# Optimization experiments

Measured on AMD Instinct MI355X. Metric: run time of the kernel, lower is better.

## Reference

```python
import jax, jax.numpy as jnp
import numpy as np

N = 50000      # num nodes
E = 800000     # num directed edges (before self loops)
C_IN = 128     # input channels
HID = 128      # hidden channels per head
H = 2          # attention heads (layer 0)
NEG_SLOPE = 0.2


def setup_inputs() -> dict:
    key = jax.random.key(0)
    ks = jax.random.split(key, 10)
    s = 0.05
    return {
        "x": jax.random.normal(ks[0], (N, C_IN), jnp.float32),
        "edge_index": jax.random.randint(ks[1], (2, E), 0, N, dtype=jnp.int32),
        "W1": jax.random.normal(ks[2], (C_IN, H * HID), jnp.float32) * s,
        "att_src1": jax.random.normal(ks[3], (H, HID), jnp.float32) * s,
        "att_dst1": jax.random.normal(ks[4], (H, HID), jnp.float32) * s,
        "b1": jax.random.normal(ks[5], (H * HID,), jnp.float32) * s,
        "W2": jax.random.normal(ks[6], (H * HID, 1), jnp.float32) * s,
        "att_src2": jax.random.normal(ks[7], (1, 1), jnp.float32) * s,
        "att_dst2": jax.random.normal(ks[8], (1, 1), jnp.float32) * s,
        "b2": jax.random.normal(ks[9], (1,), jnp.float32) * s,
    }


def gat_layer(x, src, dst, W, att_src, att_dst, bias, heads, out_ch, concat, num_nodes):
    # linear projection -> [N, H, C]
    h = (x @ W).reshape(num_nodes, heads, out_ch)
    a_src = jnp.einsum("nhc,hc->nh", h, att_src)  # [N, H]
    a_dst = jnp.einsum("nhc,hc->nh", h, att_dst)  # [N, H]
    # edge attention logits, LeakyReLU as in GATConv
    alpha = jax.nn.leaky_relu(a_src[src] + a_dst[dst], NEG_SLOPE)  # [Etot, H]
    # segment softmax over incoming edges of each destination node
    amax = jax.ops.segment_max(alpha, dst, num_segments=num_nodes)
    amax = jnp.where(jnp.isfinite(amax), amax, 0.0)
    ex = jnp.exp(alpha - amax[dst])
    denom = jax.ops.segment_sum(ex, dst, num_segments=num_nodes)
    coef = ex / (denom[dst] + 1e-16)                      # [Etot, H]
    # weighted scatter-aggregate of source features
    msg = h[src] * coef[:, :, None]                       # [Etot, H, C]
    out = jax.ops.segment_sum(msg, dst, num_segments=num_nodes)  # [N, H, C]
    out = out.reshape(num_nodes, heads * out_ch) if concat else out.mean(axis=1)
    return out + bias


def reference(x, edge_index, W1, att_src1, att_dst1, b1, W2, att_src2, att_dst2, b2):
    n = x.shape[0]
    loops = jnp.arange(n, dtype=edge_index.dtype)
    src = jnp.concatenate([edge_index[0], loops])  # GATConv adds self-loops
    dst = jnp.concatenate([edge_index[1], loops])
    h = gat_layer(x, src, dst, W1, att_src1, att_dst1, b1, H, HID, True, n)
    h = jax.nn.relu(h)
    out = gat_layer(h, src, dst, W2, att_src2, att_dst2, b2, 1, 1, False, n)
    return jax.nn.sigmoid(out)  # [N, 1]
```

## Files before the change

### kernel.cpp

```cpp
#include <hip/hip_runtime.h>
#include <hip/hip_bf16.h>

#define NEG_SLOPE 0.2f
#define MAXDEG 64

using f16x8 = __attribute__((ext_vector_type(8))) _Float16;
using f32x4 = __attribute__((ext_vector_type(4))) float;

__device__ inline unsigned short f2bf(float f) {
  __hip_bfloat16 b = __float2bfloat16(f);
  return __builtin_bit_cast(unsigned short, b);
}
__device__ inline unsigned short f2h(float f) {
  return __builtin_bit_cast(unsigned short, (_Float16)f);
}
__device__ inline float h2f(unsigned short u) {
  return (float)__builtin_bit_cast(_Float16, u);
}

__global__ __launch_bounds__(256) void k_pre(
    const float* __restrict__ W1, _Float16* __restrict__ W1T,
    int* __restrict__ cnt, int N) {
  const int b = blockIdx.x, t = threadIdx.x;
  if (b < 128) {
    const int e = b * 256 + t;
    const int k = e >> 8, c = e & 255;
    W1T[c * 128 + k] = (_Float16)W1[e];
  } else {
    const int i = (b - 128) * 256 + t;
    if (i < N) cnt[i] = 0;
  }
}

__global__ __launch_bounds__(256) void k1_mfma(
    const float* __restrict__ x, const _Float16* __restrict__ W1T,
    const float* __restrict__ att_src, const float* __restrict__ att_dst,
    _Float16* __restrict__ h1f, float4* __restrict__ attn, int N) {
  __shared__ _Float16 xs[64][136];
  const int t = threadIdx.x;
  const int w = t >> 6, l = t & 63;
  const int n0 = blockIdx.x * 64;

  {
    const int col4 = (t & 31) * 4;
#pragma unroll
    for (int p = 0; p < 8; ++p) {
      const int row = p * 8 + (t >> 5);
      float4 xv = make_float4(0.f, 0.f, 0.f, 0.f);
      if (n0 + row < N) xv = *(const float4*)(x + (size_t)(n0 + row) * 128 + col4);
      ushort4 u;
      u.x = f2h(xv.x); u.y = f2h(xv.y); u.z = f2h(xv.z); u.w = f2h(xv.w);
      *(ushort4*)&xs[row][col4] = u;
    }
  }
  __syncthreads();

  f32x4 acc[16];
#pragma unroll
  for (int nf = 0; nf < 16; ++nf) acc[nf] = f32x4{0.f, 0.f, 0.f, 0.f};
  const int cb = l & 15;
  const int kof = (l >> 4) * 8;
  const int xr = w * 16 + cb;
#pragma unroll
  for (int kk = 0; kk < 4; ++kk) {
    const f16x8 bx = *(const f16x8*)&xs[xr][kk * 32 + kof];
#pragma unroll
    for (int nf = 0; nf < 16; ++nf) {
      const f16x8 aw = *(const f16x8*)(W1T + (size_t)(nf * 16 + cb) * 128 + kk * 32 + kof);
      acc[nf] = __builtin_amdgcn_mfma_f32_16x16x32_f16(aw, bx, acc[nf], 0, 0, 0);
    }
  }

  const int node = n0 + w * 16 + cb;
  const int cg = (l >> 4) * 4;
  if (node < N) {
#pragma unroll
    for (int nf = 0; nf < 16; ++nf) {
      ushort4 u;
      u.x = f2h(acc[nf][0]); u.y = f2h(acc[nf][1]);
      u.z = f2h(acc[nf][2]); u.w = f2h(acc[nf][3]);
      *(ushort4*)(h1f + (size_t)node * 256 + nf * 16 + cg) = u;
    }
  }

  float s0 = 0.f, s1 = 0.f, d0 = 0.f, d1 = 0.f;
#pragma unroll
  for (int nf = 0; nf < 16; ++nf) {
    const float4 av = *(const float4*)(att_src + nf * 16 + cg);
    const float4 dv = *(const float4*)(att_dst + nf * 16 + cg);
    const float ls = acc[nf][0] * av.x + acc[nf][1] * av.y + acc[nf][2] * av.z + acc[nf][3] * av.w;
    const float ld = acc[nf][0] * dv.x + acc[nf][1] * dv.y + acc[nf][2] * dv.z + acc[nf][3] * dv.w;
    if (nf < 8) { s0 += ls; d0 += ld; } else { s1 += ls; d1 += ld; }
  }
  s0 += __shfl_xor(s0, 16); s0 += __shfl_xor(s0, 32);
  s1 += __shfl_xor(s1, 16); s1 += __shfl_xor(s1, 32);
  d0 += __shfl_xor(d0, 16); d0 += __shfl_xor(d0, 32);
  d1 += __shfl_xor(d1, 16); d1 += __shfl_xor(d1, 32);
  if (l < 16 && node < N) attn[node] = make_float4(s0, s1, d0, d1);
}

__global__ __launch_bounds__(256) void k_scatter(
    const int* __restrict__ ei, int E, int Etot,
    const float4* __restrict__ attn, int* __restrict__ cnt,
    int2* __restrict__ rec) {
  const int e = blockIdx.x * 256 + threadIdx.x;
  if (e >= Etot) return;
  int s, d;
  if (e < E) { s = ei[e]; d = ei[E + e]; } else { s = e - E; d = s; }
  const int slot = atomicAdd(&cnt[d], 1);
  if (slot >= MAXDEG) return;
  const float4 as = attn[s];
  const float4 ad = attn[d];
  float a0 = as.x + ad.z;
  float a1 = as.y + ad.w;
  a0 = a0 > 0.f ? a0 : a0 * NEG_SLOPE;
  a1 = a1 > 0.f ? a1 : a1 * NEG_SLOPE;
  const unsigned int wp = ((unsigned)f2bf(__expf(a1)) << 16) | f2bf(__expf(a0));
  rec[(size_t)d * MAXDEG + slot] = make_int2(s, (int)wp);
}

__global__ __launch_bounds__(256) void k3_gather(
    const int* __restrict__ cnt, const int2* __restrict__ rec,
    const _Float16* __restrict__ h1f,
    const float* __restrict__ b1, const float* __restrict__ W2,
    float* __restrict__ h2, int N) {
  const int wave = threadIdx.x >> 6, lane = threadIdx.x & 63;
  const int n = blockIdx.x * 4 + wave;
  if (n >= N) return;
  const bool hi = lane >= 32;
  const int deg = cnt[n];
  const int kcnt = deg < MAXDEG ? deg : MAXDEG;
  float4 acc = {0.f, 0.f, 0.f, 0.f};
  float den = 0.f;
  const unsigned short* h1u = (const unsigned short*)h1f;

  int sv = 0, wp = 0;
  if (lane < kcnt) {
    const int2 rv = rec[(size_t)n * MAXDEG + lane];
    sv = rv.x;
    wp = rv.y;
  }

  int s0_ = __shfl(sv, 0), s1_ = __shfl(sv, 1), s2_ = __shfl(sv, 2), s3_ = __shfl(sv, 3);
  ushort4 h0 = ((const ushort4*)(h1u + (size_t)s0_ * 256))[lane];
  ushort4 h1 = ((const ushort4*)(h1u + (size_t)s1_ * 256))[lane];
  ushort4 h2v = ((const ushort4*)(h1u + (size_t)s2_ * 256))[lane];
  ushort4 h3 = ((const ushort4*)(h1u + (size_t)s3_ * 256))[lane];

  for (int i = 0; i < kcnt; i += 4) {
    const int j0 = (i + 4) & 63, j1 = (i + 5) & 63, j2 = (i + 6) & 63, j3 = (i + 7) & 63;
    const int t0 = __shfl(sv, j0), t1 = __shfl(sv, j1), t2 = __shfl(sv, j2), t3 = __shfl(sv, j3);
    const ushort4 g0 = ((const ushort4*)(h1u + (size_t)t0 * 256))[lane];
    const ushort4 g1 = ((const ushort4*)(h1u + (size_t)t1 * 256))[lane];
    const ushort4 g2 = ((const ushort4*)(h1u + (size_t)t2 * 256))[lane];
    const ushort4 g3 = ((const ushort4*)(h1u + (size_t)t3 * 256))[lane];

    const unsigned int wp0 = (unsigned)__shfl(wp, i);
    const unsigned int wp1 = (unsigned)__shfl(wp, i + 1);
    const unsigned int wp2 = (unsigned)__shfl(wp, i + 2);
    const unsigned int wp3 = (unsigned)__shfl(wp, i + 3);
    const float w0 = __uint_as_float(hi ? (wp0 & 0xffff0000u) : (wp0 << 16));
    const float w1 = __uint_as_float(hi ? (wp1 & 0xffff0000u) : (wp1 << 16));
    const float w2 = __uint_as_float(hi ? (wp2 & 0xffff0000u) : (wp2 << 16));
    const float w3 = __uint_as_float(hi ? (wp3 & 0xffff0000u) : (wp3 << 16));

    acc.x = fmaf(h2f(h0.x), w0, acc.x); acc.y = fmaf(h2f(h0.y), w0, acc.y);
    acc.z = fmaf(h2f(h0.z), w0, acc.z); acc.w = fmaf(h2f(h0.w), w0, acc.w);
    acc.x = fmaf(h2f(h1.x), w1, acc.x); acc.y = fmaf(h2f(h1.y), w1, acc.y);
    acc.z = fmaf(h2f(h1.z), w1, acc.z); acc.w = fmaf(h2f(h1.w), w1, acc.w);
    acc.x = fmaf(h2f(h2v.x), w2, acc.x); acc.y = fmaf(h2f(h2v.y), w2, acc.y);
    acc.z = fmaf(h2f(h2v.z), w2, acc.z); acc.w = fmaf(h2f(h2v.w), w2, acc.w);
    acc.x = fmaf(h2f(h3.x), w3, acc.x); acc.y = fmaf(h2f(h3.y), w3, acc.y);
    acc.z = fmaf(h2f(h3.z), w3, acc.z); acc.w = fmaf(h2f(h3.w), w3, acc.w);
    den += w0 + w1 + w2 + w3;

    h0 = g0; h1 = g1; h2v = g2; h3 = g3;
  }

  const float inv = 1.f / (den + 1e-16f);
  const float4 bv = ((const float4*)b1)[lane];
  const float4 wv4 = ((const float4*)W2)[lane];
  float p = 0.f;
  p += fmaxf(fmaf(acc.x, inv, bv.x), 0.f) * wv4.x;
  p += fmaxf(fmaf(acc.y, inv, bv.y), 0.f) * wv4.y;
  p += fmaxf(fmaf(acc.z, inv, bv.z), 0.f) * wv4.z;
  p += fmaxf(fmaf(acc.w, inv, bv.w), 0.f) * wv4.w;
  for (int m = 32; m; m >>= 1) p += __shfl_xor(p, m);
  if (lane == 0) h2[n] = p;
}

__global__ __launch_bounds__(256) void k_l2(
    const int* __restrict__ cnt, const int2* __restrict__ rec,
    const float* __restrict__ h2,
    const float* __restrict__ att_s2, const float* __restrict__ att_d2,
    const float* __restrict__ b2, float* __restrict__ out, int N) {
  const int sub = threadIdx.x & 15;
  const int n = blockIdx.x * 16 + (threadIdx.x >> 4);
  if (n >= N) return;
  const float as2 = att_s2[0];
  const float hd = h2[n] * att_d2[0];
  const int m = min(cnt[n], MAXDEG);
  float num = 0.f, den = 0.f;
  for (int base = 0; base < m; base += 16) {
    if (base + sub < m) {
      const float hs = h2[rec[(size_t)n * MAXDEG + base + sub].x];
      float a = fmaf(hs, as2, hd);
      a = a > 0.f ? a : a * NEG_SLOPE;
      const float w = __expf(a);
      den += w;
      num = fmaf(w, hs, num);
    }
  }
  for (int mm = 8; mm; mm >>= 1) { num += __shfl_xor(num, mm); den += __shfl_xor(den, mm); }
  if (sub == 0) {
    const float v = num / (den + 1e-16f) + b2[0];
    out[n] = 1.f / (1.f + __expf(-v));
  }
}

extern "C" void kernel_launch(void* const* d_in, const int* in_sizes, int n_in,
                              void* d_out, int out_size, void* d_ws, size_t ws_size,
                              hipStream_t stream) {
  const float* x        = (const float*)d_in[0];
  const int*   ei       = (const int*)d_in[1];
  const float* W1       = (const float*)d_in[2];
  const float* att_src1 = (const float*)d_in[3];
  const float* att_dst1 = (const float*)d_in[4];
  const float* b1       = (const float*)d_in[5];
  const float* W2       = (const float*)d_in[6];
  const float* att_s2   = (const float*)d_in[7];
  const float* att_d2   = (const float*)d_in[8];
  const float* b2       = (const float*)d_in[9];
  float* out = (float*)d_out;

  const int N = in_sizes[0] / 128;
  const int E = in_sizes[1] / 2;
  const int Etot = E + N;

  char* ws = (char*)d_ws;
  size_t o = 0;
  float4* attn = (float4*)(ws + o); o += (size_t)N * 16;
  int2* rec    = (int2*)(ws + o); o += (size_t)N * MAXDEG * 8;
  _Float16* h1f = (_Float16*)(ws + o); o += (size_t)N * 256 * 2;
  _Float16* W1T = (_Float16*)(ws + o); o += (size_t)256 * 128 * 2;
  float* h2  = (float*)(ws + o); o += (size_t)N * 4;
  int* cnt   = (int*)(ws + o); o += (size_t)N * 4;

  const int nblk = (N + 255) / 256;
  k_pre<<<128 + nblk, 256, 0, stream>>>(W1, W1T, cnt, N);
  k1_mfma<<<(N + 63) / 64, 256, 0, stream>>>(x, W1T, att_src1, att_dst1, h1f, attn, N);
  k_scatter<<<(Etot + 255) / 256, 256, 0, stream>>>(ei, E, Etot, attn, cnt, rec);
  k3_gather<<<(N + 3) / 4, 256, 0, stream>>>(cnt, rec, h1f, b1, W2, h2, N);
  k_l2<<<(N + 15) / 16, 256, 0, stream>>>(cnt, rec, h2, att_s2, att_d2, b2, out, N);
}
```

Baseline: 234.9 us.

## Fuse edge scatter into GEMM launch and compute attention weights in gather

The edge bucketing (atomic slot assignment) now runs as extra blocks of the projection GEMM kernel, since it no longer depends on the attention logits. Computing the exp-weighted logits moves into the gather kernel, which reads attn[src] per lane. The record array shrinks from int2 to int, halving the scatter writes and gather reads. The cost is extra per-edge attn loads and exp work in the gather kernel, and the GEMM and scatter blocks now share one grid.

```diff
diff --git a/kernel.cpp b/kernel.cpp
--- a/kernel.cpp
+++ b/kernel.cpp
@@ -32,15 +32,30 @@
   }
 }
 
-__global__ __launch_bounds__(256) void k1_mfma(
+__global__ __launch_bounds__(256) void k_fused(
     const float* __restrict__ x, const _Float16* __restrict__ W1T,
     const float* __restrict__ att_src, const float* __restrict__ att_dst,
-    _Float16* __restrict__ h1f, float4* __restrict__ attn, int N) {
+    _Float16* __restrict__ h1f, float4* __restrict__ attn, int N,
+    const int* __restrict__ ei, int E, int Etot,
+    int* __restrict__ cnt, int* __restrict__ rec) {
   __shared__ _Float16 xs[64][136];
+  const int nGemm = (N + 63) >> 6;
+  const int b = blockIdx.x;
   const int t = threadIdx.x;
+
+  if (b >= nGemm) {
+    const int e = (b - nGemm) * 256 + t;
+    if (e < Etot) {
+      int s, d;
+      if (e < E) { s = ei[e]; d = ei[E + e]; } else { s = e - E; d = s; }
+      const int slot = atomicAdd(&cnt[d], 1);
+      if (slot < MAXDEG) rec[d * MAXDEG + slot] = s;
+    }
+    return;
+  }
+
   const int w = t >> 6, l = t & 63;
-  const int n0 = blockIdx.x * 64;
-
+  const int n0 = b * 64;
   {
     const int col4 = (t & 31) * 4;
 #pragma unroll
@@ -99,29 +114,9 @@
   if (l < 16 && node < N) attn[node] = make_float4(s0, s1, d0, d1);
 }
 
-__global__ __launch_bounds__(256) void k_scatter(
-    const int* __restrict__ ei, int E, int Etot,
-    const float4* __restrict__ attn, int* __restrict__ cnt,
-    int2* __restrict__ rec) {
-  const int e = blockIdx.x * 256 + threadIdx.x;
-  if (e >= Etot) return;
-  int s, d;
-  if (e < E) { s = ei[e]; d = ei[E + e]; } else { s = e - E; d = s; }
-  const int slot = atomicAdd(&cnt[d], 1);
-  if (slot >= MAXDEG) return;
-  const float4 as = attn[s];
-  const float4 ad = attn[d];
-  float a0 = as.x + ad.z;
-  float a1 = as.y + ad.w;
-  a0 = a0 > 0.f ? a0 : a0 * NEG_SLOPE;
-  a1 = a1 > 0.f ? a1 : a1 * NEG_SLOPE;
-  const unsigned int wp = ((unsigned)f2bf(__expf(a1)) << 16) | f2bf(__expf(a0));
-  rec[(size_t)d * MAXDEG + slot] = make_int2(s, (int)wp);
-}
-
 __global__ __launch_bounds__(256) void k3_gather(
-    const int* __restrict__ cnt, const int2* __restrict__ rec,
-    const _Float16* __restrict__ h1f,
+    const int* __restrict__ cnt, const int* __restrict__ rec,
+    const float4* __restrict__ attn, const _Float16* __restrict__ h1f,
     const float* __restrict__ b1, const float* __restrict__ W2,
     float* __restrict__ h2, int N) {
   const int wave = threadIdx.x >> 6, lane = threadIdx.x & 63;
@@ -133,12 +128,17 @@
   float4 acc = {0.f, 0.f, 0.f, 0.f};
   float den = 0.f;
   const unsigned short* h1u = (const unsigned short*)h1f;
+  const float4 an = attn[n];
 
   int sv = 0, wp = 0;
   if (lane < kcnt) {
-    const int2 rv = rec[(size_t)n * MAXDEG + lane];
-    sv = rv.x;
-    wp = rv.y;
+    sv = rec[n * MAXDEG + lane];
+    const float4 a4 = attn[sv];
+    float a0 = a4.x + an.z;
+    float a1 = a4.y + an.w;
+    a0 = a0 > 0.f ? a0 : a0 * NEG_SLOPE;
+    a1 = a1 > 0.f ? a1 : a1 * NEG_SLOPE;
+    wp = (int)(((unsigned)f2bf(__expf(a1)) << 16) | f2bf(__expf(a0)));
   }
 
   int s0_ = __shfl(sv, 0), s1_ = __shfl(sv, 1), s2_ = __shfl(sv, 2), s3_ = __shfl(sv, 3);
@@ -190,7 +190,7 @@
 }
 
 __global__ __launch_bounds__(256) void k_l2(
-    const int* __restrict__ cnt, const int2* __restrict__ rec,
+    const int* __restrict__ cnt, const int* __restrict__ rec,
     const float* __restrict__ h2,
     const float* __restrict__ att_s2, const float* __restrict__ att_d2,
     const float* __restrict__ b2, float* __restrict__ out, int N) {
@@ -203,7 +203,7 @@
   float num = 0.f, den = 0.f;
   for (int base = 0; base < m; base += 16) {
     if (base + sub < m) {
-      const float hs = h2[rec[(size_t)n * MAXDEG + base + sub].x];
+      const float hs = h2[rec[n * MAXDEG + base + sub]];
       float a = fmaf(hs, as2, hd);
       a = a > 0.f ? a : a * NEG_SLOPE;
       const float w = __expf(a);
@@ -240,16 +240,17 @@
   char* ws = (char*)d_ws;
   size_t o = 0;
   float4* attn = (float4*)(ws + o); o += (size_t)N * 16;
-  int2* rec    = (int2*)(ws + o); o += (size_t)N * MAXDEG * 8;
+  int* rec     = (int*)(ws + o); o += (size_t)N * MAXDEG * 4;
   _Float16* h1f = (_Float16*)(ws + o); o += (size_t)N * 256 * 2;
   _Float16* W1T = (_Float16*)(ws + o); o += (size_t)256 * 128 * 2;
   float* h2  = (float*)(ws + o); o += (size_t)N * 4;
   int* cnt   = (int*)(ws + o); o += (size_t)N * 4;
 
-  const int nblk = (N + 255) / 256;
-  k_pre<<<128 + nblk, 256, 0, stream>>>(W1, W1T, cnt, N);
-  k1_mfma<<<(N + 63) / 64, 256, 0, stream>>>(x, W1T, att_src1, att_dst1, h1f, attn, N);
-  k_scatter<<<(Etot + 255) / 256, 256, 0, stream>>>(ei, E, Etot, attn, cnt, rec);
-  k3_gather<<<(N + 3) / 4, 256, 0, stream>>>(cnt, rec, h1f, b1, W2, h2, N);
+  const int nGemm = (N + 63) / 64;
+  const int nScat = (Etot + 255) / 256;
+  k_pre<<<128 + (N + 255) / 256, 256, 0, stream>>>(W1, W1T, cnt, N);
+  k_fused<<<nGemm + nScat, 256, 0, stream>>>(x, W1T, att_src1, att_dst1,
+                                             h1f, attn, N, ei, E, Etot, cnt, rec);
+  k3_gather<<<(N + 3) / 4, 256, 0, stream>>>(cnt, rec, attn, h1f, b1, W2, h2, N);
   k_l2<<<(N + 15) / 16, 256, 0, stream>>>(cnt, rec, h2, att_s2, att_d2, b2, out, N);
 }
```

Measured after the change: 224.7 us. 4.3% less time.

## Fuse weight prep, GEMM, and edge scatter into one cooperative persistent kernel

Applied to the files above, without the earlier changes.

Replaces the three launches for weight transpose/counter reset, the MFMA projection and the edge scatter with one cooperative kernel that loops over work and uses grid-wide barriers between phases. The aim is to remove kernel launch gaps and tail effects between the early stages. The grid is capped at 1024 blocks sized from an occupancy query, and the original three-kernel path is kept as a fallback if the cooperative launch fails. In exchange it adds grid-sync costs, an occupancy query on the host each call, and lower parallelism in the scatter phase.

```diff
diff --git a/kernel.cpp b/kernel.cpp
--- a/kernel.cpp
+++ b/kernel.cpp
@@ -1,5 +1,8 @@
 #include <hip/hip_runtime.h>
 #include <hip/hip_bf16.h>
+#include <hip/hip_cooperative_groups.h>
+
+namespace cg = cooperative_groups;
 
 #define NEG_SLOPE 0.2f
 #define MAXDEG 64
@@ -18,29 +21,15 @@
   return (float)__builtin_bit_cast(_Float16, u);
 }
 
-__global__ __launch_bounds__(256) void k_pre(
-    const float* __restrict__ W1, _Float16* __restrict__ W1T,
-    int* __restrict__ cnt, int N) {
-  const int b = blockIdx.x, t = threadIdx.x;
-  if (b < 128) {
-    const int e = b * 256 + t;
-    const int k = e >> 8, c = e & 255;
-    W1T[c * 128 + k] = (_Float16)W1[e];
-  } else {
-    const int i = (b - 128) * 256 + t;
-    if (i < N) cnt[i] = 0;
-  }
-}
-
-__global__ __launch_bounds__(256) void k1_mfma(
-    const float* __restrict__ x, const _Float16* __restrict__ W1T,
+
+__device__ __forceinline__ void gemm_tile(
+    int tile, int t, const float* __restrict__ x, const _Float16* __restrict__ W1T,
     const float* __restrict__ att_src, const float* __restrict__ att_dst,
-    _Float16* __restrict__ h1f, float4* __restrict__ attn, int N) {
-  __shared__ _Float16 xs[64][136];
-  const int t = threadIdx.x;
+    _Float16* __restrict__ h1f, float4* __restrict__ attn, int N,
+    _Float16 (*xs)[136]) {
   const int w = t >> 6, l = t & 63;
-  const int n0 = blockIdx.x * 64;
-
+  const int n0 = tile * 64;
+  __syncthreads();
   {
     const int col4 = (t & 31) * 4;
 #pragma unroll
@@ -72,22 +61,22 @@
   }
 
   const int node = n0 + w * 16 + cb;
-  const int cg = (l >> 4) * 4;
+  const int cg_ = (l >> 4) * 4;
   if (node < N) {
 #pragma unroll
     for (int nf = 0; nf < 16; ++nf) {
       ushort4 u;
       u.x = f2h(acc[nf][0]); u.y = f2h(acc[nf][1]);
       u.z = f2h(acc[nf][2]); u.w = f2h(acc[nf][3]);
-      *(ushort4*)(h1f + (size_t)node * 256 + nf * 16 + cg) = u;
+      *(ushort4*)(h1f + (size_t)node * 256 + nf * 16 + cg_) = u;
     }
   }
 
   float s0 = 0.f, s1 = 0.f, d0 = 0.f, d1 = 0.f;
 #pragma unroll
   for (int nf = 0; nf < 16; ++nf) {
-    const float4 av = *(const float4*)(att_src + nf * 16 + cg);
-    const float4 dv = *(const float4*)(att_dst + nf * 16 + cg);
+    const float4 av = *(const float4*)(att_src + nf * 16 + cg_);
+    const float4 dv = *(const float4*)(att_dst + nf * 16 + cg_);
     const float ls = acc[nf][0] * av.x + acc[nf][1] * av.y + acc[nf][2] * av.z + acc[nf][3] * av.w;
     const float ld = acc[nf][0] * dv.x + acc[nf][1] * dv.y + acc[nf][2] * dv.z + acc[nf][3] * dv.w;
     if (nf < 8) { s0 += ls; d0 += ld; } else { s1 += ls; d1 += ld; }
@@ -99,12 +88,10 @@
   if (l < 16 && node < N) attn[node] = make_float4(s0, s1, d0, d1);
 }
 
-__global__ __launch_bounds__(256) void k_scatter(
-    const int* __restrict__ ei, int E, int Etot,
+__device__ __forceinline__ void scat_edge(
+    int e, const int* __restrict__ ei, int E,
     const float4* __restrict__ attn, int* __restrict__ cnt,
     int2* __restrict__ rec) {
-  const int e = blockIdx.x * 256 + threadIdx.x;
-  if (e >= Etot) return;
   int s, d;
   if (e < E) { s = ei[e]; d = ei[E + e]; } else { s = e - E; d = s; }
   const int slot = atomicAdd(&cnt[d], 1);
@@ -117,6 +104,65 @@
   a1 = a1 > 0.f ? a1 : a1 * NEG_SLOPE;
   const unsigned int wp = ((unsigned)f2bf(__expf(a1)) << 16) | f2bf(__expf(a0));
   rec[(size_t)d * MAXDEG + slot] = make_int2(s, (int)wp);
+}
+
+__global__ __launch_bounds__(256, 4) void k_mega(
+    const float* __restrict__ x, const float* __restrict__ W1,
+    _Float16* __restrict__ W1T,
+    const float* __restrict__ att_src, const float* __restrict__ att_dst,
+    _Float16* __restrict__ h1f, float4* __restrict__ attn, int N,
+    const int* __restrict__ ei, int E, int Etot,
+    int* __restrict__ cnt, int2* __restrict__ rec) {
+  cg::grid_group gg = cg::this_grid();
+  __shared__ _Float16 xs[64][136];
+  const int b = blockIdx.x, t = threadIdx.x, nB = gridDim.x;
+
+  for (int idx = b * 256 + t; idx < 128 * 256; idx += nB * 256) {
+    const int k = idx >> 8, c = idx & 255;
+    W1T[c * 128 + k] = (_Float16)W1[idx];
+  }
+  for (int i = b * 256 + t; i < N; i += nB * 256) cnt[i] = 0;
+  __threadfence();
+  gg.sync();
+
+  const int nGemm = (N + 63) >> 6;
+  for (int tile = b; tile < nGemm; tile += nB)
+    gemm_tile(tile, t, x, W1T, att_src, att_dst, h1f, attn, N, xs);
+  __threadfence();
+  gg.sync();
+
+  for (int e = b * 256 + t; e < Etot; e += nB * 256)
+    scat_edge(e, ei, E, attn, cnt, rec);
+}
+
+__global__ __launch_bounds__(256) void k_preF(
+    const float* __restrict__ W1, _Float16* __restrict__ W1T,
+    int* __restrict__ cnt, int N) {
+  const int b = blockIdx.x, t = threadIdx.x;
+  if (b < 128) {
+    const int e = b * 256 + t;
+    const int k = e >> 8, c = e & 255;
+    W1T[c * 128 + k] = (_Float16)W1[e];
+  } else {
+    const int i = (b - 128) * 256 + t;
+    if (i < N) cnt[i] = 0;
+  }
+}
+
+__global__ __launch_bounds__(256, 4) void k_gemmF(
+    const float* __restrict__ x, const _Float16* __restrict__ W1T,
+    const float* __restrict__ att_src, const float* __restrict__ att_dst,
+    _Float16* __restrict__ h1f, float4* __restrict__ attn, int N) {
+  __shared__ _Float16 xs[64][136];
+  gemm_tile(blockIdx.x, threadIdx.x, x, W1T, att_src, att_dst, h1f, attn, N, xs);
+}
+
+__global__ __launch_bounds__(256) void k_scatF(
+    const int* __restrict__ ei, int E, int Etot,
+    const float4* __restrict__ attn, int* __restrict__ cnt,
+    int2* __restrict__ rec) {
+  const int e = blockIdx.x * 256 + threadIdx.x;
+  if (e < Etot) scat_edge(e, ei, E, attn, cnt, rec);
 }
 
 __global__ __launch_bounds__(256) void k3_gather(
@@ -233,9 +279,9 @@
   const float* b2       = (const float*)d_in[9];
   float* out = (float*)d_out;
 
-  const int N = in_sizes[0] / 128;
-  const int E = in_sizes[1] / 2;
-  const int Etot = E + N;
+  int N = in_sizes[0] / 128;
+  int E = in_sizes[1] / 2;
+  int Etot = E + N;
 
   char* ws = (char*)d_ws;
   size_t o = 0;
@@ -246,10 +292,29 @@
   float* h2  = (float*)(ws + o); o += (size_t)N * 4;
   int* cnt   = (int*)(ws + o); o += (size_t)N * 4;
 
-  const int nblk = (N + 255) / 256;
-  k_pre<<<128 + nblk, 256, 0, stream>>>(W1, W1T, cnt, N);
-  k1_mfma<<<(N + 63) / 64, 256, 0, stream>>>(x, W1T, att_src1, att_dst1, h1f, attn, N);
-  k_scatter<<<(Etot + 255) / 256, 256, 0, stream>>>(ei, E, Etot, attn, cnt, rec);
+  int nbcu = 0;
+  hipError_t qe = hipOccupancyMaxActiveBlocksPerMultiprocessor(
+      &nbcu, reinterpret_cast<const void*>(&k_mega), 256, 0);
+  if (qe != hipSuccess || nbcu < 1) nbcu = 1;
+  int grid = nbcu * 256;
+  if (grid > 1024) grid = 1024;
+
+  void* args[] = {(void*)&x, (void*)&W1, (void*)&W1T,
+                  (void*)&att_src1, (void*)&att_dst1,
+                  (void*)&h1f, (void*)&attn, (void*)&N,
+                  (void*)&ei, (void*)&E, (void*)&Etot,
+                  (void*)&cnt, (void*)&rec};
+  hipError_t le = hipLaunchCooperativeKernel(
+      reinterpret_cast<const void*>(&k_mega), dim3(grid), dim3(256),
+      args, 0, stream);
+  if (le != hipSuccess) {
+    (void)hipGetLastError();
+    const int nGemm = (N + 63) / 64;
+    k_preF<<<128 + (N + 255) / 256, 256, 0, stream>>>(W1, W1T, cnt, N);
+    k_gemmF<<<nGemm, 256, 0, stream>>>(x, W1T, att_src1, att_dst1, h1f, attn, N);
+    k_scatF<<<(Etot + 255) / 256, 256, 0, stream>>>(ei, E, Etot, attn, cnt, rec);
+  }
+
   k3_gather<<<(N + 3) / 4, 256, 0, stream>>>(cnt, rec, h1f, b1, W2, h2, N);
   k_l2<<<(N + 15) / 16, 256, 0, stream>>>(cnt, rec, h2, att_s2, att_d2, b2, out, N);
 }
```

After: 561.2 us. +139.0%, slower.
